# Kernel tuning notes

Hardware: AMD Instinct MI355X
Metric: run time of the kernel (lower is better)

Reference implementation:

```python
import jax, jax.numpy as jnp
import numpy as np
from jax import lax

B, T, I, H = 8192, 512, 3, 25  # batch, seq_len, input_size, hidden_size


def setup_inputs() -> dict:
    key = jax.random.key(0)
    ks = jax.random.split(key, 4)
    x = jax.random.normal(ks[0], (B, T, I), dtype=jnp.float32)
    # xavier-uniform-ish scale for w_ih, orthogonal-ish (plain normal here) for w_hh
    w_ih = jax.random.normal(ks[1], (4 * H, I), dtype=jnp.float32) * 0.5
    w_hh = jax.random.normal(ks[2], (4 * H, H), dtype=jnp.float32) * 0.2
    b_ih = jnp.zeros((4 * H,), dtype=jnp.float32)
    # PyTorch init in module: forget-gate bias (second quarter) set to 1 on each bias
    b_ih = b_ih.at[H:2 * H].set(1.0)
    b_hh = jnp.zeros((4 * H,), dtype=jnp.float32)
    b_hh = b_hh.at[H:2 * H].set(1.0)
    w_lin = jax.random.normal(ks[3], (1, H), dtype=jnp.float32) * 0.3
    b_lin = jnp.zeros((1,), dtype=jnp.float32)
    return {"x": x, "w_ih": w_ih, "w_hh": w_hh, "b_ih": b_ih, "b_hh": b_hh,
            "w_lin": w_lin, "b_lin": b_lin}


def _lstm_last_h(x, w_ih, w_hh, b_ih, b_hh):
    # x: [B, T, I]; returns final hidden state h_T: [B, H]
    b = b_ih + b_hh  # [4H]
    xT = jnp.swapaxes(x, 0, 1)  # [T, B, I]

    def step(carry, x_t):
        h, c = carry
        gates = x_t @ w_ih.T + h @ w_hh.T + b  # [B, 4H]
        i, f, g, o = jnp.split(gates, 4, axis=-1)  # PyTorch gate order i,f,g,o
        i = jax.nn.sigmoid(i)
        f = jax.nn.sigmoid(f)
        g = jnp.tanh(g)
        o = jax.nn.sigmoid(o)
        c = f * c + i * g
        h = o * jnp.tanh(c)
        return (h, c), None

    h0 = jnp.zeros((x.shape[0], w_hh.shape[1]), dtype=x.dtype)
    (h, _), _ = lax.scan(step, (h0, h0), xT)
    return h


def reference(x, w_ih, w_hh, b_ih, b_hh, w_lin, b_lin):
    h_last = _lstm_last_h(x, w_ih, w_hh, b_ih, b_hh)  # [B, H]
    return h_last @ w_lin.T + b_lin  # [B, 1]
```

## Files before the change

kernel.cpp:

```cpp
#include <hip/hip_runtime.h>
#include <hip/hip_bf16.h>


#define TSTEPS 512
#define ISZ 3
#define HSZ 25
#define NTILES 512
#define NW 7
#define TSTRIDE 40

typedef __attribute__((ext_vector_type(8))) short bf16x8;
typedef __attribute__((ext_vector_type(4))) float f32x4;

__device__ __forceinline__ unsigned short bf16_bits(float v) {
    return __builtin_bit_cast(unsigned short, __float2bfloat16(v));
}
__device__ __forceinline__ unsigned int pack_bf16(float lo, float hi) {
    return ((unsigned int)bf16_bits(hi) << 16) | (unsigned int)bf16_bits(lo);
}

__device__ __forceinline__ void lstm_act(const f32x4 acc, float& c, float& h) {
    const float K1 = 1.442695040888963f;
    const float K2 = 2.885390081777927f;
    const float e0 = __builtin_amdgcn_exp2f(-K1 * acc[0]);
    const float e1 = __builtin_amdgcn_exp2f(-K1 * acc[1]);
    const float e2 = __builtin_amdgcn_exp2f(fminf(-K2 * acc[2], 126.0f));
    const float e3 = __builtin_amdgcn_exp2f(-K1 * acc[3]);
    const float f  = __builtin_amdgcn_rcpf(1.0f + e1);
    const float ig = (1.0f - e2) * __builtin_amdgcn_rcpf((1.0f + e0) * (1.0f + e2));
    c = fmaf(f, c, ig);
    const float ec = __builtin_amdgcn_exp2f(fminf(-K2 * c, 126.0f));
    h = (1.0f - ec) * __builtin_amdgcn_rcpf((1.0f + e3) * (1.0f + ec));
}

__global__ __launch_bounds__(NW * 64) void lstm_mfma(
    const float* __restrict__ x,
    const float* __restrict__ w_ih,
    const float* __restrict__ w_hh,
    const float* __restrict__ b_ih,
    const float* __restrict__ b_hh,
    const float* __restrict__ w_lin,
    const float* __restrict__ b_lin,
    float* __restrict__ out)
{
    __shared__ uint2 xpk[TSTEPS * 16];
    __shared__ short hb[2][16 * TSTRIDE];
    __shared__ float outred[NW][16];

    const int tid  = threadIdx.x;
    const int w    = tid >> 6;
    const int lane = tid & 63;
    const int n    = lane & 15;
    const int q    = lane >> 4;
    const bool isq0 = (q == 0);
    const int u    = 4 * w + q;

    for (int i = tid; i < 2 * 16 * TSTRIDE; i += NW * 64) ((short*)hb)[i] = 0;

    if (tid < 256) {
        const int bsel = tid >> 4, sub16 = tid & 15;
        const float* __restrict__ g = x + (size_t)(blockIdx.x * 16 + bsel) * (TSTEPS * ISZ);
        #pragma unroll
        for (int it = 0; it < 8; ++it) {
            const int tg = sub16 + 16 * it;
            const float4* f4 = (const float4*)(g + tg * 12);
            float4 a = f4[0], b4 = f4[1], c4 = f4[2];
            const float s[4][3] = { {a.x, a.y, a.z}, {a.w, b4.x, b4.y},
                                    {b4.z, b4.w, c4.x}, {c4.y, c4.z, c4.w} };
            #pragma unroll
            for (int uu = 0; uu < 4; ++uu) {
                uint2 d;
                d.x = pack_bf16(s[uu][0], s[uu][1]);
                d.y = pack_bf16(s[uu][2], 1.0f);
                xpk[(tg * 4 + uu) * 16 + bsel] = d;
            }
        }
    }

    bf16x8 afrag;
    #pragma unroll
    for (int j = 0; j < 8; ++j) {
        const int k = q * 8 + j;
        const int r = 16 * w + n;
        const int uu = r >> 2, g = r & 3;
        float v = 0.0f;
        if (uu < HSZ) {
            const int orow = g * HSZ + uu;
            if (k < ISZ)            v = w_ih[orow * ISZ + k];
            else if (k == ISZ)      v = b_ih[orow] + b_hh[orow];
            else if (k < 4 + HSZ)   v = w_hh[orow * HSZ + (k - 4)];
        }
        afrag[j] = (short)bf16_bits(v);
    }

    __syncthreads();

    float c = 0.f, h = 0.f;
    uint2 xdw = xpk[n];

    #pragma unroll 1
    for (int t = 0; t < TSTEPS; ++t) {
        const int tn = (t + 1 < TSTEPS) ? t + 1 : t;
        const uint2 xnxt = xpk[tn * 16 + n];

        const short* __restrict__ rrow = &hb[t & 1][n * TSTRIDE];
        short* __restrict__ wrow = &hb[(t + 1) & 1][n * TSTRIDE];

        bf16x8 bfrag = *reinterpret_cast<const bf16x8*>(rrow + q * 8);
        {
            uint4 bi = __builtin_bit_cast(uint4, bfrag);
            if (isq0) { bi.x = xdw.x; bi.y = xdw.y; }
            bfrag = __builtin_bit_cast(bf16x8, bi);
        }

        const f32x4 acc = __builtin_amdgcn_mfma_f32_16x16x32_bf16(
            afrag, bfrag, (f32x4){0.f, 0.f, 0.f, 0.f}, 0, 0, 0);

        lstm_act(acc, c, h);

        if (w < 6 || isq0)
            wrow[4 + u] = (short)bf16_bits(h);

        xdw = xnxt;
        __syncthreads();
    }

    float v = 0.f;
    if (w < 6 || isq0) v = w_lin[u] * h;
    v += __shfl_xor(v, 16);
    v += __shfl_xor(v, 32);
    if (lane < 16) outred[w][lane] = v;
    __syncthreads();
    if (tid < 16) {
        float s = b_lin[0];
        #pragma unroll
        for (int k = 0; k < NW; ++k) s += outred[k][tid];
        out[blockIdx.x * 16 + tid] = s;
    }
}

extern "C" void kernel_launch(void* const* d_in, const int* in_sizes, int n_in,
                              void* d_out, int out_size, void* d_ws, size_t ws_size,
                              hipStream_t stream) {
    const float* x     = (const float*)d_in[0];
    const float* w_ih  = (const float*)d_in[1];
    const float* w_hh  = (const float*)d_in[2];
    const float* b_ih  = (const float*)d_in[3];
    const float* b_hh  = (const float*)d_in[4];
    const float* w_lin = (const float*)d_in[5];
    const float* b_lin = (const float*)d_in[6];
    float* out = (float*)d_out;

    lstm_mfma<<<NTILES, NW * 64, 0, stream>>>(x, w_ih, w_hh, b_ih, b_hh,
                                              w_lin, b_lin, out);
}
```

Baseline: 301.6 us.

## Interleave two independent batch tiles per block to hide recurrence latency

```diff
diff --git a/kernel.cpp b/kernel.cpp
--- a/kernel.cpp
+++ b/kernel.cpp
@@ -5,8 +5,8 @@
 #define TSTEPS 512
 #define ISZ 3
 #define HSZ 25
-#define NTILES 512
 #define NW 7
+#define CHUNK 256
 #define TSTRIDE 40
 
 typedef __attribute__((ext_vector_type(8))) short bf16x8;
@@ -43,9 +43,9 @@
     const float* __restrict__ b_lin,
     float* __restrict__ out)
 {
-    __shared__ uint2 xpk[TSTEPS * 16];
-    __shared__ short hb[2][16 * TSTRIDE];
-    __shared__ float outred[NW][16];
+    __shared__ uint2 xpk[2][CHUNK][16];
+    __shared__ short hb[2][2][16 * TSTRIDE];
+    __shared__ float outred[2][NW][16];
 
     const int tid  = threadIdx.x;
     const int w    = tid >> 6;
@@ -54,15 +54,16 @@
     const int q    = lane >> 4;
     const bool isq0 = (q == 0);
     const int u    = 4 * w + q;
+    const bool act = (w < 6) || isq0;
 
-    for (int i = tid; i < 2 * 16 * TSTRIDE; i += NW * 64) ((short*)hb)[i] = 0;
+    for (int i = tid; i < 2 * 2 * 16 * TSTRIDE; i += NW * 64) ((short*)hb)[i] = 0;
 
-    if (tid < 256) {
-        const int bsel = tid >> 4, sub16 = tid & 15;
-        const float* __restrict__ g = x + (size_t)(blockIdx.x * 16 + bsel) * (TSTEPS * ISZ);
-        #pragma unroll
-        for (int it = 0; it < 8; ++it) {
-            const int tg = sub16 + 16 * it;
+    auto stage = [&](int c0) {
+        const int bsel = tid & 31;
+        const int tile = bsel >> 4, nn = bsel & 15;
+        const float* __restrict__ g =
+            x + (size_t)(blockIdx.x * 32 + bsel) * (TSTEPS * ISZ) + c0 * ISZ;
+        for (int tg = tid >> 5; tg < CHUNK / 4; tg += 14) {
             const float4* f4 = (const float4*)(g + tg * 12);
             float4 a = f4[0], b4 = f4[1], c4 = f4[2];
             const float s[4][3] = { {a.x, a.y, a.z}, {a.w, b4.x, b4.y},
@@ -72,10 +73,11 @@
                 uint2 d;
                 d.x = pack_bf16(s[uu][0], s[uu][1]);
                 d.y = pack_bf16(s[uu][2], 1.0f);
-                xpk[(tg * 4 + uu) * 16 + bsel] = d;
+                xpk[tile][tg * 4 + uu][nn] = d;
             }
         }
-    }
+    };
+    stage(0);
 
     bf16x8 afrag;
     #pragma unroll
@@ -95,47 +97,56 @@
 
     __syncthreads();
 
-    float c = 0.f, h = 0.f;
-    uint2 xdw = xpk[n];
+    float cA = 0.f, hA = 0.f, cB = 0.f, hB = 0.f;
+    bf16x8 bfA = *reinterpret_cast<const bf16x8*>(&hb[0][0][n * TSTRIDE + q * 8]);
 
     #pragma unroll 1
     for (int t = 0; t < TSTEPS; ++t) {
-        const int tn = (t + 1 < TSTEPS) ? t + 1 : t;
-        const uint2 xnxt = xpk[tn * 16 + n];
+        if (t == CHUNK) {
+            stage(CHUNK);
+            __syncthreads();
+        }
+        const int ts = t & (CHUNK - 1);
+        const uint2 xA = xpk[0][ts][n];
+        const uint2 xB = xpk[1][ts][n];
+        bf16x8 bfB = *reinterpret_cast<const bf16x8*>(&hb[t & 1][1][n * TSTRIDE + q * 8]);
 
-        const short* __restrict__ rrow = &hb[t & 1][n * TSTRIDE];
-        short* __restrict__ wrow = &hb[(t + 1) & 1][n * TSTRIDE];
+        {
+            uint4 bi = __builtin_bit_cast(uint4, bfA);
+            if (isq0) { bi.x = xA.x; bi.y = xA.y; }
+            const f32x4 accA = __builtin_amdgcn_mfma_f32_16x16x32_bf16(
+                afrag, __builtin_bit_cast(bf16x8, bi),
+                (f32x4){0.f, 0.f, 0.f, 0.f}, 0, 0, 0);
+            lstm_act(accA, cA, hA);
+            if (act) hb[(t + 1) & 1][0][n * TSTRIDE + 4 + u] = (short)bf16_bits(hA);
+        }
+        __syncthreads();
+        bfA = *reinterpret_cast<const bf16x8*>(&hb[(t + 1) & 1][0][n * TSTRIDE + q * 8]);
 
-        bf16x8 bfrag = *reinterpret_cast<const bf16x8*>(rrow + q * 8);
         {
-            uint4 bi = __builtin_bit_cast(uint4, bfrag);
-            if (isq0) { bi.x = xdw.x; bi.y = xdw.y; }
-            bfrag = __builtin_bit_cast(bf16x8, bi);
+            uint4 bi = __builtin_bit_cast(uint4, bfB);
+            if (isq0) { bi.x = xB.x; bi.y = xB.y; }
+            const f32x4 accB = __builtin_amdgcn_mfma_f32_16x16x32_bf16(
+                afrag, __builtin_bit_cast(bf16x8, bi),
+                (f32x4){0.f, 0.f, 0.f, 0.f}, 0, 0, 0);
+            lstm_act(accB, cB, hB);
+            if (act) hb[(t + 1) & 1][1][n * TSTRIDE + 4 + u] = (short)bf16_bits(hB);
         }
-
-        const f32x4 acc = __builtin_amdgcn_mfma_f32_16x16x32_bf16(
-            afrag, bfrag, (f32x4){0.f, 0.f, 0.f, 0.f}, 0, 0, 0);
-
-        lstm_act(acc, c, h);
-
-        if (w < 6 || isq0)
-            wrow[4 + u] = (short)bf16_bits(h);
-
-        xdw = xnxt;
         __syncthreads();
     }
 
-    float v = 0.f;
-    if (w < 6 || isq0) v = w_lin[u] * h;
-    v += __shfl_xor(v, 16);
-    v += __shfl_xor(v, 32);
-    if (lane < 16) outred[w][lane] = v;
+    float vA = 0.f, vB = 0.f;
+    if (act) { vA = w_lin[u] * hA; vB = w_lin[u] * hB; }
+    vA += __shfl_xor(vA, 16); vA += __shfl_xor(vA, 32);
+    vB += __shfl_xor(vB, 16); vB += __shfl_xor(vB, 32);
+    if (lane < 16) { outred[0][w][lane] = vA; outred[1][w][lane] = vB; }
     __syncthreads();
-    if (tid < 16) {
+    if (tid < 32) {
+        const int tile = tid >> 4, nn = tid & 15;
         float s = b_lin[0];
         #pragma unroll
-        for (int k = 0; k < NW; ++k) s += outred[k][tid];
-        out[blockIdx.x * 16 + tid] = s;
+        for (int k = 0; k < NW; ++k) s += outred[tile][k][nn];
+        out[blockIdx.x * 32 + tile * 16 + nn] = s;
     }
 }
 
@@ -151,6 +162,6 @@
     const float* b_lin = (const float*)d_in[6];
     float* out = (float*)d_out;
 
-    lstm_mfma<<<NTILES, NW * 64, 0, stream>>>(x, w_ih, w_hh, b_ih, b_hh,
-                                              w_lin, b_lin, out);
+    lstm_mfma<<<8192 / 32, NW * 64, 0, stream>>>(x, w_ih, w_hh, b_ih, b_hh,
+                                                 w_lin, b_lin, out);
 }
```

Result: slower. 345.7 us (+14.6%).

## Stage x in two LDS chunks and inject x into h buffer via idle lanes

Applied to the files above, without the earlier changes.

```diff
diff --git a/kernel.cpp b/kernel.cpp
--- a/kernel.cpp
+++ b/kernel.cpp
@@ -5,8 +5,8 @@
 #define TSTEPS 512
 #define ISZ 3
 #define HSZ 25
-#define NTILES 512
 #define NW 7
+#define CHUNK 256
 #define TSTRIDE 40
 
 typedef __attribute__((ext_vector_type(8))) short bf16x8;
@@ -43,7 +43,7 @@
     const float* __restrict__ b_lin,
     float* __restrict__ out)
 {
-    __shared__ uint2 xpk[TSTEPS * 16];
+    __shared__ uint2 xpk[CHUNK][16];
     __shared__ short hb[2][16 * TSTRIDE];
     __shared__ float outred[NW][16];
 
@@ -52,30 +52,35 @@
     const int lane = tid & 63;
     const int n    = lane & 15;
     const int q    = lane >> 4;
-    const bool isq0 = (q == 0);
     const int u    = 4 * w + q;
+    const bool actm = (w < 6) || (q == 0);
+    const bool isxw = (w == 6) && (q == 1);
 
     for (int i = tid; i < 2 * 16 * TSTRIDE; i += NW * 64) ((short*)hb)[i] = 0;
 
-    if (tid < 256) {
-        const int bsel = tid >> 4, sub16 = tid & 15;
-        const float* __restrict__ g = x + (size_t)(blockIdx.x * 16 + bsel) * (TSTEPS * ISZ);
-        #pragma unroll
-        for (int it = 0; it < 8; ++it) {
-            const int tg = sub16 + 16 * it;
-            const float4* f4 = (const float4*)(g + tg * 12);
-            float4 a = f4[0], b4 = f4[1], c4 = f4[2];
-            const float s[4][3] = { {a.x, a.y, a.z}, {a.w, b4.x, b4.y},
-                                    {b4.z, b4.w, c4.x}, {c4.y, c4.z, c4.w} };
+    auto stage = [&](int c0) {
+        if (tid < 256) {
+            const int bsel = tid >> 4, sub16 = tid & 15;
+            const float* __restrict__ g =
+                x + (size_t)(blockIdx.x * 16 + bsel) * (TSTEPS * ISZ) + c0 * ISZ;
             #pragma unroll
-            for (int uu = 0; uu < 4; ++uu) {
-                uint2 d;
-                d.x = pack_bf16(s[uu][0], s[uu][1]);
-                d.y = pack_bf16(s[uu][2], 1.0f);
-                xpk[(tg * 4 + uu) * 16 + bsel] = d;
+            for (int it = 0; it < 4; ++it) {
+                const int tg = sub16 + 16 * it;
+                const float4* f4 = (const float4*)(g + tg * 12);
+                float4 a = f4[0], b4 = f4[1], c4 = f4[2];
+                const float s[4][3] = { {a.x, a.y, a.z}, {a.w, b4.x, b4.y},
+                                        {b4.z, b4.w, c4.x}, {c4.y, c4.z, c4.w} };
+                #pragma unroll
+                for (int uu = 0; uu < 4; ++uu) {
+                    uint2 d;
+                    d.x = pack_bf16(s[uu][0], s[uu][1]);
+                    d.y = pack_bf16(s[uu][2], 1.0f);
+                    xpk[tg * 4 + uu][bsel] = d;
+                }
             }
         }
-    }
+    };
+    stage(0);
 
     bf16x8 afrag;
     #pragma unroll
@@ -94,39 +99,39 @@
     }
 
     __syncthreads();
+    if (isxw) *(uint2*)&hb[0][n * TSTRIDE] = xpk[0][n];
+    __syncthreads();
 
     float c = 0.f, h = 0.f;
-    uint2 xdw = xpk[n];
+    const int rdoff = n * TSTRIDE + q * 8;
+    const int wroff = n * TSTRIDE + 4 + u;
+    const int xwoff = n * TSTRIDE;
+
+    auto step = [&](int t, short* __restrict__ rb, short* __restrict__ wb) {
+        const bf16x8 bfrag = *reinterpret_cast<const bf16x8*>(rb + rdoff);
+        const f32x4 acc = __builtin_amdgcn_mfma_f32_16x16x32_bf16(
+            afrag, bfrag, (f32x4){0.f, 0.f, 0.f, 0.f}, 0, 0, 0);
+        lstm_act(acc, c, h);
+        if (actm) wb[wroff] = (short)bf16_bits(h);
+        if (isxw) *(uint2*)&wb[xwoff] = xpk[(t + 1) & (CHUNK - 1)][n];
+        __syncthreads();
+    };
 
     #pragma unroll 1
-    for (int t = 0; t < TSTEPS; ++t) {
-        const int tn = (t + 1 < TSTEPS) ? t + 1 : t;
-        const uint2 xnxt = xpk[tn * 16 + n];
-
-        const short* __restrict__ rrow = &hb[t & 1][n * TSTRIDE];
-        short* __restrict__ wrow = &hb[(t + 1) & 1][n * TSTRIDE];
-
-        bf16x8 bfrag = *reinterpret_cast<const bf16x8*>(rrow + q * 8);
-        {
-            uint4 bi = __builtin_bit_cast(uint4, bfrag);
-            if (isq0) { bi.x = xdw.x; bi.y = xdw.y; }
-            bfrag = __builtin_bit_cast(bf16x8, bi);
+    for (int t = 0; t < TSTEPS; t += 2) {
+        if (t == CHUNK - 2) {
+            step(t, hb[0], hb[1]);
+            stage(CHUNK);
+            __syncthreads();
+            step(t + 1, hb[1], hb[0]);
+            continue;
         }
-
-        const f32x4 acc = __builtin_amdgcn_mfma_f32_16x16x32_bf16(
-            afrag, bfrag, (f32x4){0.f, 0.f, 0.f, 0.f}, 0, 0, 0);
-
-        lstm_act(acc, c, h);
-
-        if (w < 6 || isq0)
-            wrow[4 + u] = (short)bf16_bits(h);
-
-        xdw = xnxt;
-        __syncthreads();
+        step(t, hb[0], hb[1]);
+        step(t + 1, hb[1], hb[0]);
     }
 
     float v = 0.f;
-    if (w < 6 || isq0) v = w_lin[u] * h;
+    if (actm) v = w_lin[u] * h;
     v += __shfl_xor(v, 16);
     v += __shfl_xor(v, 32);
     if (lane < 16) outred[w][lane] = v;
@@ -151,6 +156,6 @@
     const float* b_lin = (const float*)d_in[6];
     float* out = (float*)d_out;
 
-    lstm_mfma<<<NTILES, NW * 64, 0, stream>>>(x, w_ih, w_hh, b_ih, b_hh,
-                                              w_lin, b_lin, out);
+    lstm_mfma<<<8192 / 16, NW * 64, 0, stream>>>(x, w_ih, w_hh, b_ih, b_hh,
+                                                 w_lin, b_lin, out);
 }
```

Result: faster. 269.0 us (-10.8%).
